# Kernel optimization log

Measured on AMD Instinct MI355X. Metric: run time of the kernel, lower is better.

## Reference

```python
import jax, jax.numpy as jnp
import numpy as np

EMBED_DIM = 1024
NUM_HEADS = 16
HEAD_DIM = EMBED_DIM // NUM_HEADS
SCALING = HEAD_DIM ** -0.5
EPS = 1e-5


def _rope(seq_len):
    inv_freq = 1.0 / (10000.0 ** (jnp.arange(0, HEAD_DIM, 2, dtype=jnp.float32) / HEAD_DIM))
    freqs = jnp.arange(seq_len, dtype=jnp.float32)[:, None] * inv_freq[None, :]
    emb = jnp.concatenate([freqs, freqs], axis=-1)  # (S, HEAD_DIM)
    return jnp.cos(emb), jnp.sin(emb)


def _rotate(x, cos, sin):
    # x: (B,H,S,Dh), cos/sin: (S,Dh)
    d = x.shape[-1]
    x1, x2 = x[..., : d // 2], x[..., d // 2 :]
    rotated = jnp.concatenate([-x2, x1], axis=-1)
    return x * cos + rotated * sin


def setup_inputs() -> dict:
    key = jax.random.key(0)
    ks = jax.random.split(key, 6)
    B, S, D = 2, 2048, EMBED_DIM
    scale = D ** -0.5
    return {
        "x": jax.random.normal(ks[0], (B, S, D), jnp.float32),
        "Wq": jax.random.normal(ks[1], (D, D), jnp.float32) * scale,
        "Wk": jax.random.normal(ks[2], (D, D), jnp.float32) * scale,
        "Wv": jax.random.normal(ks[3], (D, D), jnp.float32) * scale,
        "Wg": jax.random.normal(ks[4], (D, D), jnp.float32) * scale,
        "Wo": jax.random.normal(ks[5], (D, D), jnp.float32) * scale,
        "gn_w": jnp.ones((D,), jnp.float32),
        "gn_b": jnp.zeros((D,), jnp.float32),
    }


def reference(x, Wq, Wk, Wv, Wg, Wo, gn_w, gn_b):
    B, S, D = x.shape
    H, Dh = NUM_HEADS, HEAD_DIM

    def split_heads(t):  # (B,S,D) -> (B,H,S,Dh)
        return t.reshape(B, S, H, Dh).transpose(0, 2, 1, 3)

    q = split_heads(x @ Wq.T)
    k = split_heads(x @ Wk.T)
    v = split_heads(x @ Wv.T)

    cos, sin = _rope(S)
    q = _rotate(q, cos, sin)
    k = _rotate(k, cos, sin)

    retention = jnp.einsum("bhsd,bhtd->bhst", q, k) * SCALING

    # multiplicative causal decay mask: gamma**(n-m) for n>=m else 0
    gammas = (1.0 - 2.0 ** (-5.0 - jnp.arange(H, dtype=jnp.float32)))  # (H,)
    diff = jnp.arange(S)[:, None] - jnp.arange(S)[None, :]             # (S,S)
    causal = diff >= 0
    decay = jnp.where(causal, gammas[:, None, None] ** jnp.maximum(diff, 0).astype(jnp.float32), 0.0)  # (H,S,S)
    retention = retention * decay[None]

    out = jnp.einsum("bhst,bhtd->bhsd", retention, v)  # (B,H,S,Dh)
    out = out.transpose(0, 2, 1, 3).reshape(B * S, H, Dh)

    # GroupNorm with num_groups == H over channel dim D
    mean = out.mean(axis=-1, keepdims=True)
    var = out.var(axis=-1, keepdims=True)
    out = (out - mean) * jax.lax.rsqrt(var + EPS)
    out = out * gn_w.reshape(H, Dh) + gn_b.reshape(H, Dh)
    out = out.reshape(B, S, D)

    gate = jax.nn.silu(x @ Wg.T)
    return (gate * out) @ Wo.T
```

## Files before the change

### kernel.cpp

```cpp
#include <hip/hip_runtime.h>
#include <cstdint>
#include <cstddef>


typedef __attribute__((ext_vector_type(4))) float  f32x4;
typedef __attribute__((ext_vector_type(8))) short  bf16x8;
typedef __attribute__((ext_vector_type(4))) short  bf16x4v;
typedef __attribute__((ext_vector_type(2))) unsigned int u32x2;

#define MFMA_BF16 __builtin_amdgcn_mfma_f32_16x16x32_bf16

#define GLL16(gp, lp) __builtin_amdgcn_global_load_lds( \
    (const __attribute__((address_space(1))) unsigned int*)(const void*)(gp), \
    (__attribute__((address_space(3))) unsigned int*)(void*)(lp), 16, 0, 0)

__device__ __forceinline__ unsigned short f2bf(float f) {
    unsigned u = __float_as_uint(f);
    u += 0x7fffu + ((u >> 16) & 1u);
    return (unsigned short)(u >> 16);
}
__device__ __forceinline__ float bf2f(unsigned short h) {
    return __uint_as_float(((unsigned)h) << 16);
}
__device__ __forceinline__ unsigned cvt_pk_bf16(float lo, float hi) {
    unsigned r;
    asm("v_cvt_pk_bf16_f32 %0, %1, %2" : "=v"(r) : "v"(lo), "v"(hi));
    return r;
}

__global__ void convert_kernel(const float* __restrict__ x,
                               const float* __restrict__ wq, const float* __restrict__ wk,
                               const float* __restrict__ wv, const float* __restrict__ wg,
                               const float* __restrict__ wo,
                               unsigned short* __restrict__ dst) {
    const size_t total = 4194304u + 5u * 1048576u;
    for (size_t i = (size_t)blockIdx.x * blockDim.x + threadIdx.x;
         i * 4 < total; i += (size_t)gridDim.x * blockDim.x) {
        size_t e = i * 4;
        const float* src; size_t off;
        if (e < 4194304u) { src = x; off = e; }
        else {
            size_t r = e - 4194304u;
            int w = (int)(r >> 20); off = r & 1048575u;
            src = (w == 0) ? wq : (w == 1) ? wk : (w == 2) ? wv : (w == 3) ? wg : wo;
        }
        f32x4 v = *(const f32x4*)(src + off);
        unsigned short o0 = f2bf(v[0]), o1 = f2bf(v[1]), o2 = f2bf(v[2]), o3 = f2bf(v[3]);
        unsigned long long pack = (unsigned long long)o0 | ((unsigned long long)o1 << 16)
                                | ((unsigned long long)o2 << 32) | ((unsigned long long)o3 << 48);
        *(unsigned long long*)(dst + e) = pack;
    }
}

__global__ void rope_tables(float* __restrict__ cosT, float* __restrict__ sinT) {
    int i = blockIdx.x * blockDim.x + threadIdx.x;
    if (i >= 2048 * 32) return;
    int s = i >> 5, j = i & 31;
    float inv = exp2f(-(float)j * (13.287712379549449f / 32.0f));
    float ang = (float)s * inv;
    cosT[i] = cosf(ang);
    sinT[i] = sinf(ang);
}

__launch_bounds__(256, 2)
__global__ void gemm_fused(const unsigned short* __restrict__ A_x,
                           const unsigned short* __restrict__ A_a2,
                           const unsigned short* __restrict__ Wq, const unsigned short* __restrict__ Wk,
                           const unsigned short* __restrict__ Wv, const unsigned short* __restrict__ Wg,
                           const unsigned short* __restrict__ Wo,
                           const float* __restrict__ cosT, const float* __restrict__ sinT,
                           unsigned short* __restrict__ q_hm, unsigned short* __restrict__ k_hm,
                           unsigned short* __restrict__ kTs, unsigned short* __restrict__ vT,
                           unsigned short* __restrict__ gate,
                           float* __restrict__ outf,
                           int mode_base) {
    int mode = mode_base + blockIdx.z;
    const unsigned short* A = (mode == 4) ? A_a2 : A_x;
    const unsigned short* W = (mode == 0) ? Wq : (mode == 1) ? Wk :
                              (mode == 2) ? Wv : (mode == 3) ? Wg : Wo;

    __shared__ __align__(16) unsigned short Ash[128 * 64];
    __shared__ __align__(16) unsigned short Bsh[128 * 64];

    int tid = threadIdx.x;
    int lane = tid & 63, wid = tid >> 6;
    int wm = wid >> 1, wn = wid & 1;
    int m0 = blockIdx.y * 128, n0 = blockIdx.x * 128;

    int l_row = lane >> 3;
    int l_src = ((lane & 7) ^ l_row) << 3;
    const unsigned short* Ab = A + (size_t)(m0 + wid * 32 + l_row) * 1024 + l_src;
    const unsigned short* Wb = W + (size_t)(n0 + wid * 32 + l_row) * 1024 + l_src;

    f32x4 acc[4][4];
#pragma unroll
    for (int i = 0; i < 4; ++i)
#pragma unroll
        for (int j = 0; j < 4; ++j)
#pragma unroll
            for (int r = 0; r < 4; ++r) acc[i][j][r] = 0.0f;

    for (int k0 = 0; k0 < 1024; k0 += 64) {
        __syncthreads();
#pragma unroll
        for (int i = 0; i < 4; ++i) {
            GLL16(Ab + (size_t)(i * 8) * 1024 + k0, &Ash[(wid * 32 + i * 8) * 64]);
            GLL16(Wb + (size_t)(i * 8) * 1024 + k0, &Bsh[(wid * 32 + i * 8) * 64]);
        }
        __syncthreads();
#pragma unroll
        for (int ks = 0; ks < 2; ++ks) {
            bf16x8 af[4], bfv[4];
#pragma unroll
            for (int mi = 0; mi < 4; ++mi) {
                int row = wm * 64 + mi * 16 + (lane & 15);
                int c = ks * 4 + (lane >> 4);
                af[mi] = *(const bf16x8*)&Ash[row * 64 + ((c ^ (row & 7)) << 3)];
            }
#pragma unroll
            for (int ni = 0; ni < 4; ++ni) {
                int row = wn * 64 + ni * 16 + (lane & 15);
                int c = ks * 4 + (lane >> 4);
                bfv[ni] = *(const bf16x8*)&Bsh[row * 64 + ((c ^ (row & 7)) << 3)];
            }
            if (mode == 2) {
#pragma unroll
                for (int mi = 0; mi < 4; ++mi)
#pragma unroll
                    for (int ni = 0; ni < 4; ++ni)
                        acc[mi][ni] = MFMA_BF16(bfv[ni], af[mi], acc[mi][ni], 0, 0, 0);
            } else {
#pragma unroll
                for (int mi = 0; mi < 4; ++mi)
#pragma unroll
                    for (int ni = 0; ni < 4; ++ni)
                        acc[mi][ni] = MFMA_BF16(af[mi], bfv[ni], acc[mi][ni], 0, 0, 0);
            }
        }
    }

    int mbase = m0 + wm * 64, nbase = n0 + wn * 64;
    int g4 = (lane >> 4) << 2;

    if (mode == 0 || mode == 1) {
        unsigned short* dst = (mode == 0) ? q_hm : k_hm;
        float sr[4] = {1.f, 1.f, 1.f, 1.f}, m16p[4] = {1.f, 1.f, 1.f, 1.f};
        if (mode == 1) {
            float lg = log2f(1.0f - exp2f(-5.0f - (float)(nbase >> 6)));
            float gm1 = exp2f(-lg), gm16 = exp2f(-16.0f * lg);
            sr[0] = exp2f(lg * (float)(63 - g4));
            sr[1] = sr[0] * gm1; sr[2] = sr[1] * gm1; sr[3] = sr[2] * gm1;
            m16p[1] = gm16; m16p[2] = gm16 * gm16; m16p[3] = m16p[2] * gm16;
        }
#pragma unroll
        for (int mi = 0; mi < 4; ++mi)
#pragma unroll
            for (int ni = 0; ni < 4; ++ni)
#pragma unroll
                for (int r = 0; r < 4; ++r) {
                    int m = mbase + mi * 16 + g4 + r;
                    int n = nbase + ni * 16 + (lane & 15);
                    int s = m & 2047, b = m >> 11, h = n >> 6, d = n & 63, j = d & 31;
                    float v  = acc[mi][ni][r];
                    float v2 = acc[mi][ni ^ 2][r];
                    float cs = cosT[s * 32 + j], sn = sinT[s * 32 + j];
                    float rot = (d < 32) ? -v2 : v2;
                    float o = v * cs + rot * sn;
                    dst[((size_t)(b * 16 + h) * 2048 + s) * 64 + d] = f2bf(o);
                    if (mode == 1) {
                        kTs[((size_t)((b * 16 + h) * 64 + d)) * 2048 + s]
                            = f2bf(o * (sr[r] * m16p[mi]));
                    }
                }
    } else if (mode == 2) {
#pragma unroll
        for (int mi = 0; mi < 4; ++mi)
#pragma unroll
            for (int ni = 0; ni < 4; ++ni)
#pragma unroll
                for (int r = 0; r < 4; ++r) {
                    int n = nbase + ni * 16 + g4 + r;
                    int m = mbase + mi * 16 + (lane & 15);
                    int b = m >> 11, s = m & 2047, h = n >> 6, d = n & 63;
                    vT[((size_t)((b * 16 + h) * 64 + d)) * 2048 + s] = f2bf(acc[mi][ni][r]);
                }
    } else if (mode == 3) {
#pragma unroll
        for (int mi = 0; mi < 4; ++mi)
#pragma unroll
            for (int ni = 0; ni < 4; ++ni)
#pragma unroll
                for (int r = 0; r < 4; ++r) {
                    int m = mbase + mi * 16 + g4 + r;
                    int n = nbase + ni * 16 + (lane & 15);
                    float v = acc[mi][ni][r];
                    gate[(size_t)m * 1024 + n] = f2bf(v / (1.0f + expf(-v)));
                }
    } else {
#pragma unroll
        for (int mi = 0; mi < 4; ++mi)
#pragma unroll
            for (int ni = 0; ni < 4; ++ni)
#pragma unroll
                for (int r = 0; r < 4; ++r) {
                    int m = mbase + mi * 16 + g4 + r;
                    int n = nbase + ni * 16 + (lane & 15);
                    outf[(size_t)m * 1024 + n] = acc[mi][ni][r];
                }
    }
}

__launch_bounds__(256, 4)
__global__ void chunk_state_kernel(const unsigned short* __restrict__ vT,
                                   const unsigned short* __restrict__ kTs,
                                   unsigned short* __restrict__ LT) {
    int tid = threadIdx.x, lane = tid & 63, wid = tid >> 6;
    int bh = blockIdx.x >> 3;
    int c  = (blockIdx.x & 7) * 4 + wid;
    int q_lane = lane & 15;
    int g4 = (lane >> 4) << 2, g8 = (lane >> 4) << 3;

    const unsigned short* vb = vT  + (size_t)bh * 131072 + (size_t)c * 64;
    const unsigned short* kb = kTs + (size_t)bh * 131072 + (size_t)c * 64;

    f32x4 acc[4][4];
#pragma unroll
    for (int i = 0; i < 4; ++i)
#pragma unroll
        for (int j = 0; j < 4; ++j)
#pragma unroll
            for (int r = 0; r < 4; ++r) acc[i][j][r] = 0.0f;

#pragma unroll
    for (int ks = 0; ks < 2; ++ks) {
        bf16x8 a[4], bv[4];
#pragma unroll
        for (int mi = 0; mi < 4; ++mi)
            a[mi] = *(const bf16x8*)(vb + (size_t)(mi * 16 + q_lane) * 2048 + ks * 32 + g8);
#pragma unroll
        for (int ni = 0; ni < 4; ++ni)
            bv[ni] = *(const bf16x8*)(kb + (size_t)(ni * 16 + q_lane) * 2048 + ks * 32 + g8);
#pragma unroll
        for (int mi = 0; mi < 4; ++mi)
#pragma unroll
            for (int ni = 0; ni < 4; ++ni)
                acc[mi][ni] = MFMA_BF16(a[mi], bv[ni], acc[mi][ni], 0, 0, 0);
    }

    unsigned short* lp = LT + ((size_t)(bh * 32 + c)) * 4096;
#pragma unroll
    for (int mi = 0; mi < 4; ++mi)
#pragma unroll
        for (int ni = 0; ni < 4; ++ni)
#pragma unroll
            for (int r = 0; r < 4; ++r) {
                int d2 = mi * 16 + g4 + r;
                int d1 = ni * 16 + q_lane;
                lp[d2 * 64 + d1] = f2bf(acc[mi][ni][r]);
            }
}

__launch_bounds__(256, 4)
__global__ void scan_kernel(const unsigned short* __restrict__ LT,
                            unsigned short* __restrict__ ST) {
    int bh = blockIdx.x >> 2;
    int e0 = ((blockIdx.x & 3) * 256 + threadIdx.x) * 4;
    int h = bh & 15;
    float lg2g = log2f(1.0f - exp2f(-5.0f - (float)h));
    float g64 = exp2f(64.0f * lg2g);

    float s0 = 0.f, s1 = 0.f, s2 = 0.f, s3 = 0.f;
    const unsigned short* lp = LT + (size_t)bh * 32 * 4096 + e0;
    unsigned short* sp = ST + (size_t)bh * 32 * 4096 + e0;
    for (int c = 0; c < 32; ++c) {
        u32x2 wv;
        wv[0] = cvt_pk_bf16(s0, s1);
        wv[1] = cvt_pk_bf16(s2, s3);
        *(u32x2*)sp = wv;
        bf16x4v lv = *(const bf16x4v*)lp;
        s0 = s0 * g64 + bf2f((unsigned short)lv[0]);
        s1 = s1 * g64 + bf2f((unsigned short)lv[1]);
        s2 = s2 * g64 + bf2f((unsigned short)lv[2]);
        s3 = s3 * g64 + bf2f((unsigned short)lv[3]);
        lp += 4096; sp += 4096;
    }
}

__launch_bounds__(256, 4)
__global__ void retention_chunk_kernel(const unsigned short* __restrict__ qh,
                                       const unsigned short* __restrict__ kh,
                                       const unsigned short* __restrict__ vT,
                                       const unsigned short* __restrict__ ST,
                                       const float* __restrict__ gn_w, const float* __restrict__ gn_b,
                                       const unsigned short* __restrict__ gate,
                                       unsigned short* __restrict__ a2) {
    __shared__ __align__(16) unsigned short Ssh[4][16 * 40];

    int tid = threadIdx.x, lane = tid & 63, wid = tid >> 6;
    int c = blockIdx.x, bh = blockIdx.y;
    int b = bh >> 4, h = bh & 15;

    float lg2g = log2f(1.0f - exp2f(-5.0f - (float)h));
    float gam1 = exp2f(lg2g);
    float gmr1 = exp2f(-lg2g);
    float gmr2 = gmr1 * gmr1, gmr3 = gmr2 * gmr1;
    float gmr16 = exp2f(-16.0f * lg2g);

    int q_lane = lane & 15;
    int g4 = (lane >> 4) << 2, g8 = (lane >> 4) << 3;
    int i_col = wid * 16 + q_lane;
    int s_abs = c * 64 + i_col;

    bf16x8 aq0, aq1;
    {
        const unsigned short* qp = qh + ((size_t)bh * 2048 + s_abs) * 64 + g8;
        aq0 = *(const bf16x8*)(qp);
        aq1 = *(const bf16x8*)(qp + 32);
    }

    f32x4 z4 = {0.f, 0.f, 0.f, 0.f};
    f32x4 o0, o1, o2, o3;

    {
        const unsigned short* stp = ST + ((size_t)(bh * 32 + c)) * 4096
                                  + (size_t)q_lane * 64 + g8;
        bf16x8 s00 = *(const bf16x8*)(stp);
        bf16x8 s01 = *(const bf16x8*)(stp + 32);
        bf16x8 s10 = *(const bf16x8*)(stp + 1024);
        bf16x8 s11 = *(const bf16x8*)(stp + 1056);
        bf16x8 s20 = *(const bf16x8*)(stp + 2048);
        bf16x8 s21 = *(const bf16x8*)(stp + 2080);
        bf16x8 s30 = *(const bf16x8*)(stp + 3072);
        bf16x8 s31 = *(const bf16x8*)(stp + 3104);
        o0 = MFMA_BF16(aq0, s00, z4, 0, 0, 0); o0 = MFMA_BF16(aq1, s01, o0, 0, 0, 0);
        o1 = MFMA_BF16(aq0, s10, z4, 0, 0, 0); o1 = MFMA_BF16(aq1, s11, o1, 0, 0, 0);
        o2 = MFMA_BF16(aq0, s20, z4, 0, 0, 0); o2 = MFMA_BF16(aq1, s21, o2, 0, 0, 0);
        o3 = MFMA_BF16(aq0, s30, z4, 0, 0, 0); o3 = MFMA_BF16(aq1, s31, o3, 0, 0, 0);
    }
    {
        float cs0 = 0.125f * exp2f(lg2g * (float)(wid * 16 + g4 + 1));
        float cs1 = cs0 * gam1, cs2 = cs1 * gam1, cs3 = cs2 * gam1;
        o0[0] *= cs0; o0[1] *= cs1; o0[2] *= cs2; o0[3] *= cs3;
        o1[0] *= cs0; o1[1] *= cs1; o1[2] *= cs2; o1[3] *= cs3;
        o2[0] *= cs0; o2[1] *= cs1; o2[2] *= cs2; o2[3] *= cs3;
        o3[0] *= cs0; o3[1] *= cs1; o3[2] *= cs2; o3[3] *= cs3;
    }

    const unsigned short* kbase = kh + ((size_t)bh * 2048 + c * 64) * 64;
    const unsigned short* vbase = vT + (size_t)bh * 131072 + c * 64;
    unsigned short* ssw = &Ssh[wid][0];
    int ntt = (wid >> 1) + 1;
    for (int tt = 0; tt < ntt; ++tt) {
        int tbase = tt * 32;
        const unsigned short* kp = kbase + (size_t)(tbase + q_lane) * 64 + g8;
        bf16x8 k00 = *(const bf16x8*)(kp);
        bf16x8 k01 = *(const bf16x8*)(kp + 32);
        bf16x8 k10 = *(const bf16x8*)(kp + 1024);
        bf16x8 k11 = *(const bf16x8*)(kp + 1056);
        f32x4 sc0 = z4, sc1 = z4;
        sc0 = MFMA_BF16(k00, aq0, sc0, 0, 0, 0);
        sc0 = MFMA_BF16(k01, aq1, sc0, 0, 0, 0);
        sc1 = MFMA_BF16(k10, aq0, sc1, 0, 0, 0);
        sc1 = MFMA_BF16(k11, aq1, sc1, 0, 0, 0);

        int j0 = tbase + g4;
        float e0 = 0.125f * exp2f(lg2g * (float)(i_col - j0));
        float e1 = e0 * gmr1, e2 = e0 * gmr2, e3 = e0 * gmr3;
        float v00 = (i_col >= j0    ) ? sc0[0] * e0 : 0.0f;
        float v01 = (i_col >= j0 + 1) ? sc0[1] * e1 : 0.0f;
        float v02 = (i_col >= j0 + 2) ? sc0[2] * e2 : 0.0f;
        float v03 = (i_col >= j0 + 3) ? sc0[3] * e3 : 0.0f;
        int j1 = j0 + 16;
        float f0 = e0 * gmr16, f1 = e1 * gmr16, f2 = e2 * gmr16, f3 = e3 * gmr16;
        float v10 = (i_col >= j1    ) ? sc1[0] * f0 : 0.0f;
        float v11 = (i_col >= j1 + 1) ? sc1[1] * f1 : 0.0f;
        float v12 = (i_col >= j1 + 2) ? sc1[2] * f2 : 0.0f;
        float v13 = (i_col >= j1 + 3) ? sc1[3] * f3 : 0.0f;

        u32x2 wA, wB;
        wA[0] = cvt_pk_bf16(v00, v01); wA[1] = cvt_pk_bf16(v02, v03);
        wB[0] = cvt_pk_bf16(v10, v11); wB[1] = cvt_pk_bf16(v12, v13);
        *(u32x2*)&ssw[q_lane * 40 + g4] = wA;
        *(u32x2*)&ssw[q_lane * 40 + 16 + g4] = wB;

        bf16x8 sf = *(const bf16x8*)&ssw[q_lane * 40 + g8];
        bf16x8 bv0 = *(const bf16x8*)(vbase + (size_t)(q_lane) * 2048 + tbase + g8);
        bf16x8 bv1 = *(const bf16x8*)(vbase + (size_t)(16 + q_lane) * 2048 + tbase + g8);
        bf16x8 bv2 = *(const bf16x8*)(vbase + (size_t)(32 + q_lane) * 2048 + tbase + g8);
        bf16x8 bv3 = *(const bf16x8*)(vbase + (size_t)(48 + q_lane) * 2048 + tbase + g8);
        o0 = MFMA_BF16(sf, bv0, o0, 0, 0, 0);
        o1 = MFMA_BF16(sf, bv1, o1, 0, 0, 0);
        o2 = MFMA_BF16(sf, bv2, o2, 0, 0, 0);
        o3 = MFMA_BF16(sf, bv3, o3, 0, 0, 0);
    }

    float mean[4], rstd[4];
#pragma unroll
    for (int r = 0; r < 4; ++r) {
        float s1 = o0[r] + o1[r] + o2[r] + o3[r];
        float s2 = o0[r]*o0[r] + o1[r]*o1[r] + o2[r]*o2[r] + o3[r]*o3[r];
#pragma unroll
        for (int m = 1; m < 16; m <<= 1) {
            s1 += __shfl_xor(s1, m);
            s2 += __shfl_xor(s2, m);
        }
        float mu = s1 * 0.015625f;
        mean[r] = mu;
        float var = s2 * 0.015625f - mu * mu;
        rstd[r] = rsqrtf(var + 1e-5f);
    }
    int srow = c * 64 + wid * 16;
#define RT_STORE(OV, DB)                                                    \
    {                                                                       \
        int d = DB * 16 + q_lane;                                           \
        float gw = gn_w[h * 64 + d];                                        \
        float gb = gn_b[h * 64 + d];                                        \
        _Pragma("unroll")                                                   \
        for (int r = 0; r < 4; ++r) {                                       \
            int s_out = srow + g4 + r;                                      \
            size_t gi = ((size_t)(b * 2048 + s_out)) * 1024 + h * 64 + d;   \
            float val = (OV[r] - mean[r]) * rstd[r] * gw + gb;              \
            val *= bf2f(gate[gi]);                                          \
            a2[gi] = f2bf(val);                                             \
        }                                                                   \
    }
    RT_STORE(o0, 0); RT_STORE(o1, 1); RT_STORE(o2, 2); RT_STORE(o3, 3);
#undef RT_STORE
}

extern "C" void kernel_launch(void* const* d_in, const int* in_sizes, int n_in,
                              void* d_out, int out_size, void* d_ws, size_t ws_size,
                              hipStream_t stream) {
    const float* x    = (const float*)d_in[0];
    const float* Wq   = (const float*)d_in[1];
    const float* Wk   = (const float*)d_in[2];
    const float* Wv   = (const float*)d_in[3];
    const float* Wg   = (const float*)d_in[4];
    const float* Wo   = (const float*)d_in[5];
    const float* gn_w = (const float*)d_in[6];
    const float* gn_b = (const float*)d_in[7];

    unsigned short* xb   = (unsigned short*)d_ws;
    unsigned short* wqb  = xb  + 4194304;
    unsigned short* wkb  = wqb + 1048576;
    unsigned short* wvb  = wkb + 1048576;
    unsigned short* wgb  = wvb + 1048576;
    unsigned short* wob  = wgb + 1048576;
    float*          cosT = (float*)(wob + 1048576);
    float*          sinT = cosT + 65536;
    unsigned short* q_hm = (unsigned short*)(sinT + 65536);
    unsigned short* k_hm = q_hm + 4194304;
    unsigned short* vTb  = k_hm + 4194304;
    unsigned short* kTs  = vTb + 4194304;
    unsigned short* a2   = kTs + 4194304;
    unsigned short* gate = a2  + 4194304;
    unsigned short* LT   = a2;
    unsigned short* ST   = xb;

    float* outf = (float*)d_out;

    convert_kernel<<<dim3(2048), dim3(256), 0, stream>>>(x, Wq, Wk, Wv, Wg, Wo, xb);
    rope_tables<<<dim3(256), dim3(256), 0, stream>>>(cosT, sinT);
    gemm_fused<<<dim3(8, 32, 4), dim3(256), 0, stream>>>(
        xb, a2, wqb, wkb, wvb, wgb, wob, cosT, sinT,
        q_hm, k_hm, kTs, vTb, gate, outf, 0);
    chunk_state_kernel<<<dim3(256), dim3(256), 0, stream>>>(vTb, kTs, LT);
    scan_kernel<<<dim3(128), dim3(256), 0, stream>>>(LT, ST);
    retention_chunk_kernel<<<dim3(32, 32), dim3(256), 0, stream>>>(
        q_hm, k_hm, vTb, ST, gn_w, gn_b, gate, a2);
    gemm_fused<<<dim3(8, 32, 1), dim3(256), 0, stream>>>(
        xb, a2, wqb, wkb, wvb, wgb, wob, cosT, sinT,
        q_hm, k_hm, kTs, vTb, gate, outf, 4);
}
```

Measured before the change: 120.3 us.

## Double-buffer GEMM LDS tiles and fold rope table generation into convert kernel

The projection GEMM now ping-pongs two LDS buffers, so the global-to-LDS loads for the next K tile are issued before the MFMAs on the current tile, and there is one barrier per iteration instead of two. MFMA sections are wrapped in s_setprio to favour the math waves. Separately, the rope cos/sin table computation moves into the first 256 blocks of the convert kernel, which removes one kernel launch. Doubling LDS to 64KB per block may limit how many blocks fit per CU alongside the launch bound of 2.

After: 120.2 us, median of 2. Within noise of the previous version (-0.1%).

```diff
diff --git a/kernel.cpp b/kernel.cpp
--- a/kernel.cpp
+++ b/kernel.cpp
@@ -32,7 +32,8 @@
                                const float* __restrict__ wq, const float* __restrict__ wk,
                                const float* __restrict__ wv, const float* __restrict__ wg,
                                const float* __restrict__ wo,
-                               unsigned short* __restrict__ dst) {
+                               unsigned short* __restrict__ dst,
+                               float* __restrict__ cosT, float* __restrict__ sinT) {
     const size_t total = 4194304u + 5u * 1048576u;
     for (size_t i = (size_t)blockIdx.x * blockDim.x + threadIdx.x;
          i * 4 < total; i += (size_t)gridDim.x * blockDim.x) {
@@ -50,16 +51,14 @@
                                 | ((unsigned long long)o2 << 32) | ((unsigned long long)o3 << 48);
         *(unsigned long long*)(dst + e) = pack;
     }
-}
-
-__global__ void rope_tables(float* __restrict__ cosT, float* __restrict__ sinT) {
-    int i = blockIdx.x * blockDim.x + threadIdx.x;
-    if (i >= 2048 * 32) return;
-    int s = i >> 5, j = i & 31;
-    float inv = exp2f(-(float)j * (13.287712379549449f / 32.0f));
-    float ang = (float)s * inv;
-    cosT[i] = cosf(ang);
-    sinT[i] = sinf(ang);
+    if (blockIdx.x < 256) {
+        int i = blockIdx.x * 256 + threadIdx.x;
+        int s = i >> 5, j = i & 31;
+        float inv = exp2f(-(float)j * (13.287712379549449f / 32.0f));
+        float ang = (float)s * inv;
+        cosT[i] = cosf(ang);
+        sinT[i] = sinf(ang);
+    }
 }
 
 __launch_bounds__(256, 2)
@@ -79,8 +78,8 @@
     const unsigned short* W = (mode == 0) ? Wq : (mode == 1) ? Wk :
                               (mode == 2) ? Wv : (mode == 3) ? Wg : Wo;
 
-    __shared__ __align__(16) unsigned short Ash[128 * 64];
-    __shared__ __align__(16) unsigned short Bsh[128 * 64];
+    __shared__ __align__(16) unsigned short Ash[2][128 * 64];
+    __shared__ __align__(16) unsigned short Bsh[2][128 * 64];
 
     int tid = threadIdx.x;
     int lane = tid & 63, wid = tid >> 6;
@@ -100,44 +99,61 @@
 #pragma unroll
             for (int r = 0; r < 4; ++r) acc[i][j][r] = 0.0f;
 
-    for (int k0 = 0; k0 < 1024; k0 += 64) {
+#define STAGE(BUF, K0)                                                          \
+    _Pragma("unroll")                                                           \
+    for (int i_ = 0; i_ < 4; ++i_) {                                            \
+        GLL16(Ab + (size_t)(i_ * 8) * 1024 + (K0), &Ash[BUF][(wid * 32 + i_ * 8) * 64]); \
+        GLL16(Wb + (size_t)(i_ * 8) * 1024 + (K0), &Bsh[BUF][(wid * 32 + i_ * 8) * 64]); \
+    }
+
+#define COMPUTE(BUF)                                                            \
+    _Pragma("unroll")                                                           \
+    for (int ks = 0; ks < 2; ++ks) {                                            \
+        bf16x8 af[4], bfv[4];                                                   \
+        _Pragma("unroll")                                                       \
+        for (int mi = 0; mi < 4; ++mi) {                                        \
+            int row = wm * 64 + mi * 16 + (lane & 15);                          \
+            int c = ks * 4 + (lane >> 4);                                       \
+            af[mi] = *(const bf16x8*)&Ash[BUF][row * 64 + ((c ^ (row & 7)) << 3)]; \
+        }                                                                       \
+        _Pragma("unroll")                                                       \
+        for (int ni = 0; ni < 4; ++ni) {                                        \
+            int row = wn * 64 + ni * 16 + (lane & 15);                          \
+            int c = ks * 4 + (lane >> 4);                                       \
+            bfv[ni] = *(const bf16x8*)&Bsh[BUF][row * 64 + ((c ^ (row & 7)) << 3)]; \
+        }                                                                       \
+        __builtin_amdgcn_s_setprio(1);                                          \
+        if (mode == 2) {                                \
+            _Pragma("unroll")                                                   \
+            for (int mi = 0; mi < 4; ++mi)                                      \
+                _Pragma("unroll")                                               \
+                for (int ni = 0; ni < 4; ++ni)                                  \
+                    acc[mi][ni] = MFMA_BF16(bfv[ni], af[mi], acc[mi][ni], 0, 0, 0); \
+        } else {                                                                \
+            _Pragma("unroll")                                                   \
+            for (int mi = 0; mi < 4; ++mi)                                      \
+                _Pragma("unroll")                                               \
+                for (int ni = 0; ni < 4; ++ni)                                  \
+                    acc[mi][ni] = MFMA_BF16(af[mi], bfv[ni], acc[mi][ni], 0, 0, 0); \
+        }                                                                       \
+        __builtin_amdgcn_s_setprio(0);                                          \
+    }
+
+    STAGE(0, 0)
+    asm volatile("s_waitcnt vmcnt(0)" ::: "memory");
+    __syncthreads();
+
+    for (int t = 0; t < 15; ++t) {
+        int cur = t & 1;
+        STAGE(cur ^ 1, (t + 1) * 64)
+        COMPUTE(cur)
+        asm volatile("s_waitcnt vmcnt(0)" ::: "memory");
         __syncthreads();
-#pragma unroll
-        for (int i = 0; i < 4; ++i) {
-            GLL16(Ab + (size_t)(i * 8) * 1024 + k0, &Ash[(wid * 32 + i * 8) * 64]);
-            GLL16(Wb + (size_t)(i * 8) * 1024 + k0, &Bsh[(wid * 32 + i * 8) * 64]);
-        }
-        __syncthreads();
-#pragma unroll
-        for (int ks = 0; ks < 2; ++ks) {
-            bf16x8 af[4], bfv[4];
-#pragma unroll
-            for (int mi = 0; mi < 4; ++mi) {
-                int row = wm * 64 + mi * 16 + (lane & 15);
-                int c = ks * 4 + (lane >> 4);
-                af[mi] = *(const bf16x8*)&Ash[row * 64 + ((c ^ (row & 7)) << 3)];
-            }
-#pragma unroll
-            for (int ni = 0; ni < 4; ++ni) {
-                int row = wn * 64 + ni * 16 + (lane & 15);
-                int c = ks * 4 + (lane >> 4);
-                bfv[ni] = *(const bf16x8*)&Bsh[row * 64 + ((c ^ (row & 7)) << 3)];
-            }
-            if (mode == 2) {
-#pragma unroll
-                for (int mi = 0; mi < 4; ++mi)
-#pragma unroll
-                    for (int ni = 0; ni < 4; ++ni)
-                        acc[mi][ni] = MFMA_BF16(bfv[ni], af[mi], acc[mi][ni], 0, 0, 0);
-            } else {
-#pragma unroll
-                for (int mi = 0; mi < 4; ++mi)
-#pragma unroll
-                    for (int ni = 0; ni < 4; ++ni)
-                        acc[mi][ni] = MFMA_BF16(af[mi], bfv[ni], acc[mi][ni], 0, 0, 0);
-            }
-        }
-    }
+    }
+    COMPUTE(1)
+
+#undef STAGE
+#undef COMPUTE
 
     int mbase = m0 + wm * 64, nbase = n0 + wn * 64;
     int g4 = (lane >> 4) << 2;
@@ -459,8 +475,8 @@
 
     float* outf = (float*)d_out;
 
-    convert_kernel<<<dim3(2048), dim3(256), 0, stream>>>(x, Wq, Wk, Wv, Wg, Wo, xb);
-    rope_tables<<<dim3(256), dim3(256), 0, stream>>>(cosT, sinT);
+    convert_kernel<<<dim3(2048), dim3(256), 0, stream>>>(
+        x, Wq, Wk, Wv, Wg, Wo, xb, cosT, sinT);
     gemm_fused<<<dim3(8, 32, 4), dim3(256), 0, stream>>>(
         xb, a2, wqb, wkb, wvb, wgb, wob, cosT, sinT,
         q_hm, k_hm, kTs, vTb, gate, outf, 0);
```

## Double-buffer GEMM LDS loads, remap workgroups, and use narrower tiles for output projection

Applied to the files above, without the earlier changes.

The GEMM now double-buffers its LDS tiles, so global-to-LDS loads for the next K step are issued while MFMAs run on the current one, and it raises wave priority around the MFMA block. Workgroup indices are remapped flat across groups of eight, likely to spread neighbouring tiles across XCDs for better cache locality. The output projection uses a templated 128x64 tile with a 512-workgroup grid for better CU occupancy. The rope table computation is folded into the convert kernel to save a launch. Double buffering doubles LDS use, which can lower occupancy.

Result: slower. 132.3 us (+9.9%).

```diff
diff --git a/kernel.cpp b/kernel.cpp
--- a/kernel.cpp
+++ b/kernel.cpp
@@ -32,7 +32,8 @@
                                const float* __restrict__ wq, const float* __restrict__ wk,
                                const float* __restrict__ wv, const float* __restrict__ wg,
                                const float* __restrict__ wo,
-                               unsigned short* __restrict__ dst) {
+                               unsigned short* __restrict__ dst,
+                               float* __restrict__ cosT, float* __restrict__ sinT) {
     const size_t total = 4194304u + 5u * 1048576u;
     for (size_t i = (size_t)blockIdx.x * blockDim.x + threadIdx.x;
          i * 4 < total; i += (size_t)gridDim.x * blockDim.x) {
@@ -50,19 +51,18 @@
                                 | ((unsigned long long)o2 << 32) | ((unsigned long long)o3 << 48);
         *(unsigned long long*)(dst + e) = pack;
     }
-}
-
-__global__ void rope_tables(float* __restrict__ cosT, float* __restrict__ sinT) {
-    int i = blockIdx.x * blockDim.x + threadIdx.x;
-    if (i >= 2048 * 32) return;
-    int s = i >> 5, j = i & 31;
-    float inv = exp2f(-(float)j * (13.287712379549449f / 32.0f));
-    float ang = (float)s * inv;
-    cosT[i] = cosf(ang);
-    sinT[i] = sinf(ang);
-}
-
-__launch_bounds__(256, 2)
+    if (blockIdx.x < 256) {
+        int i = blockIdx.x * 256 + threadIdx.x;
+        int s = i >> 5, j = i & 31;
+        float inv = exp2f(-(float)j * (13.287712379549449f / 32.0f));
+        float ang = (float)s * inv;
+        cosT[i] = cosf(ang);
+        sinT[i] = sinf(ang);
+    }
+}
+
+template<int NI>
+__launch_bounds__(256, NI == 4 ? 2 : 3)
 __global__ void gemm_fused(const unsigned short* __restrict__ A_x,
                            const unsigned short* __restrict__ A_a2,
                            const unsigned short* __restrict__ Wq, const unsigned short* __restrict__ Wk,
@@ -74,133 +74,167 @@
                            unsigned short* __restrict__ gate,
                            float* __restrict__ outf,
                            int mode_base) {
-    int mode = mode_base + blockIdx.z;
+    constexpr int BROWS = NI * 32;
+
+    int flat = (blockIdx.z * gridDim.y + blockIdx.y) * gridDim.x + blockIdx.x;
+    int nwg  = gridDim.z * gridDim.y * gridDim.x;
+    int L    = (flat & 7) * (nwg >> 3) + (flat >> 3);
+
+    int mode, m0, n0;
+    if (NI == 4) {
+        mode = mode_base + (L >> 8);
+        int rem = L & 255;
+        m0 = (rem >> 3) * 128;
+        n0 = (rem & 7) * 128;
+    } else {
+        mode = mode_base;
+        m0 = (L >> 4) * 128;
+        n0 = (L & 15) * 64;
+    }
+
     const unsigned short* A = (mode == 4) ? A_a2 : A_x;
     const unsigned short* W = (mode == 0) ? Wq : (mode == 1) ? Wk :
                               (mode == 2) ? Wv : (mode == 3) ? Wg : Wo;
 
-    __shared__ __align__(16) unsigned short Ash[128 * 64];
-    __shared__ __align__(16) unsigned short Bsh[128 * 64];
+    __shared__ __align__(16) unsigned short Ash[2][128 * 64];
+    __shared__ __align__(16) unsigned short Bsh[2][BROWS * 64];
 
     int tid = threadIdx.x;
     int lane = tid & 63, wid = tid >> 6;
     int wm = wid >> 1, wn = wid & 1;
-    int m0 = blockIdx.y * 128, n0 = blockIdx.x * 128;
 
     int l_row = lane >> 3;
     int l_src = ((lane & 7) ^ l_row) << 3;
     const unsigned short* Ab = A + (size_t)(m0 + wid * 32 + l_row) * 1024 + l_src;
-    const unsigned short* Wb = W + (size_t)(n0 + wid * 32 + l_row) * 1024 + l_src;
-
-    f32x4 acc[4][4];
+    const unsigned short* Wb = W + (size_t)(n0 + wid * (BROWS / 4) + l_row) * 1024 + l_src;
+
+    f32x4 acc[4][NI];
 #pragma unroll
     for (int i = 0; i < 4; ++i)
 #pragma unroll
-        for (int j = 0; j < 4; ++j)
+        for (int j = 0; j < NI; ++j)
 #pragma unroll
             for (int r = 0; r < 4; ++r) acc[i][j][r] = 0.0f;
 
-    for (int k0 = 0; k0 < 1024; k0 += 64) {
-        __syncthreads();
-#pragma unroll
-        for (int i = 0; i < 4; ++i) {
-            GLL16(Ab + (size_t)(i * 8) * 1024 + k0, &Ash[(wid * 32 + i * 8) * 64]);
-            GLL16(Wb + (size_t)(i * 8) * 1024 + k0, &Bsh[(wid * 32 + i * 8) * 64]);
-        }
-        __syncthreads();
+    auto stage = [&](int buf, int k0) {
+#pragma unroll
+        for (int i = 0; i < 4; ++i)
+            GLL16(Ab + (size_t)(i * 8) * 1024 + k0, &Ash[buf][(wid * 32 + i * 8) * 64]);
+#pragma unroll
+        for (int i = 0; i < NI; ++i)
+            GLL16(Wb + (size_t)(i * 8) * 1024 + k0, &Bsh[buf][(wid * (BROWS / 4) + i * 8) * 64]);
+    };
+
+    auto compute = [&](int buf) {
 #pragma unroll
         for (int ks = 0; ks < 2; ++ks) {
-            bf16x8 af[4], bfv[4];
+            bf16x8 af[4], bfv[NI];
+            int c = ks * 4 + (lane >> 4);
 #pragma unroll
             for (int mi = 0; mi < 4; ++mi) {
                 int row = wm * 64 + mi * 16 + (lane & 15);
-                int c = ks * 4 + (lane >> 4);
-                af[mi] = *(const bf16x8*)&Ash[row * 64 + ((c ^ (row & 7)) << 3)];
+                af[mi] = *(const bf16x8*)&Ash[buf][row * 64 + ((c ^ (row & 7)) << 3)];
             }
 #pragma unroll
-            for (int ni = 0; ni < 4; ++ni) {
-                int row = wn * 64 + ni * 16 + (lane & 15);
-                int c = ks * 4 + (lane >> 4);
-                bfv[ni] = *(const bf16x8*)&Bsh[row * 64 + ((c ^ (row & 7)) << 3)];
+            for (int ni = 0; ni < NI; ++ni) {
+                int row = wn * (BROWS / 2) + ni * 16 + (lane & 15);
+                bfv[ni] = *(const bf16x8*)&Bsh[buf][row * 64 + ((c ^ (row & 7)) << 3)];
             }
+            __builtin_amdgcn_s_setprio(1);
             if (mode == 2) {
 #pragma unroll
                 for (int mi = 0; mi < 4; ++mi)
 #pragma unroll
-                    for (int ni = 0; ni < 4; ++ni)
+                    for (int ni = 0; ni < NI; ++ni)
                         acc[mi][ni] = MFMA_BF16(bfv[ni], af[mi], acc[mi][ni], 0, 0, 0);
             } else {
 #pragma unroll
                 for (int mi = 0; mi < 4; ++mi)
 #pragma unroll
-                    for (int ni = 0; ni < 4; ++ni)
+                    for (int ni = 0; ni < NI; ++ni)
                         acc[mi][ni] = MFMA_BF16(af[mi], bfv[ni], acc[mi][ni], 0, 0, 0);
             }
+            __builtin_amdgcn_s_setprio(0);
         }
-    }
-
-    int mbase = m0 + wm * 64, nbase = n0 + wn * 64;
+    };
+
+    stage(0, 0);
+    asm volatile("s_waitcnt vmcnt(0)" ::: "memory");
+    __syncthreads();
+
+    for (int t = 0; t < 15; ++t) {
+        int cur = t & 1;
+        stage(cur ^ 1, (t + 1) * 64);
+        compute(cur);
+        asm volatile("s_waitcnt vmcnt(0)" ::: "memory");
+        __syncthreads();
+    }
+    compute(1);
+
+    int mbase = m0 + wm * 64, nbase = n0 + wn * (BROWS / 2);
     int g4 = (lane >> 4) << 2;
 
-    if (mode == 0 || mode == 1) {
-        unsigned short* dst = (mode == 0) ? q_hm : k_hm;
-        float sr[4] = {1.f, 1.f, 1.f, 1.f}, m16p[4] = {1.f, 1.f, 1.f, 1.f};
-        if (mode == 1) {
-            float lg = log2f(1.0f - exp2f(-5.0f - (float)(nbase >> 6)));
-            float gm1 = exp2f(-lg), gm16 = exp2f(-16.0f * lg);
-            sr[0] = exp2f(lg * (float)(63 - g4));
-            sr[1] = sr[0] * gm1; sr[2] = sr[1] * gm1; sr[3] = sr[2] * gm1;
-            m16p[1] = gm16; m16p[2] = gm16 * gm16; m16p[3] = m16p[2] * gm16;
+    if constexpr (NI == 4) {
+        if (mode == 0 || mode == 1) {
+            unsigned short* dst = (mode == 0) ? q_hm : k_hm;
+            float sr[4] = {1.f, 1.f, 1.f, 1.f}, m16p[4] = {1.f, 1.f, 1.f, 1.f};
+            if (mode == 1) {
+                float lg = log2f(1.0f - exp2f(-5.0f - (float)(nbase >> 6)));
+                float gm1 = exp2f(-lg), gm16 = exp2f(-16.0f * lg);
+                sr[0] = exp2f(lg * (float)(63 - g4));
+                sr[1] = sr[0] * gm1; sr[2] = sr[1] * gm1; sr[3] = sr[2] * gm1;
+                m16p[1] = gm16; m16p[2] = gm16 * gm16; m16p[3] = m16p[2] * gm16;
+            }
+#pragma unroll
+            for (int mi = 0; mi < 4; ++mi)
+#pragma unroll
+                for (int ni = 0; ni < 4; ++ni)
+#pragma unroll
+                    for (int r = 0; r < 4; ++r) {
+                        int m = mbase + mi * 16 + g4 + r;
+                        int n = nbase + ni * 16 + (lane & 15);
+                        int s = m & 2047, b = m >> 11, h = n >> 6, d = n & 63, j = d & 31;
+                        float v  = acc[mi][ni][r];
+                        float v2 = acc[mi][ni ^ 2][r];
+                        float cs = cosT[s * 32 + j], sn = sinT[s * 32 + j];
+                        float rot = (d < 32) ? -v2 : v2;
+                        float o = v * cs + rot * sn;
+                        dst[((size_t)(b * 16 + h) * 2048 + s) * 64 + d] = f2bf(o);
+                        if (mode == 1) {
+                            kTs[((size_t)((b * 16 + h) * 64 + d)) * 2048 + s]
+                                = f2bf(o * (sr[r] * m16p[mi]));
+                        }
+                    }
+        } else if (mode == 2) {
+#pragma unroll
+            for (int mi = 0; mi < 4; ++mi)
+#pragma unroll
+                for (int ni = 0; ni < 4; ++ni)
+#pragma unroll
+                    for (int r = 0; r < 4; ++r) {
+                        int n = nbase + ni * 16 + g4 + r;
+                        int m = mbase + mi * 16 + (lane & 15);
+                        int b = m >> 11, s = m & 2047, h = n >> 6, d = n & 63;
+                        vT[((size_t)((b * 16 + h) * 64 + d)) * 2048 + s] = f2bf(acc[mi][ni][r]);
+                    }
+        } else {
+#pragma unroll
+            for (int mi = 0; mi < 4; ++mi)
+#pragma unroll
+                for (int ni = 0; ni < 4; ++ni)
+#pragma unroll
+                    for (int r = 0; r < 4; ++r) {
+                        int m = mbase + mi * 16 + g4 + r;
+                        int n = nbase + ni * 16 + (lane & 15);
+                        float v = acc[mi][ni][r];
+                        gate[(size_t)m * 1024 + n] = f2bf(v / (1.0f + expf(-v)));
+                    }
         }
+    } else {
 #pragma unroll
         for (int mi = 0; mi < 4; ++mi)
 #pragma unroll
-            for (int ni = 0; ni < 4; ++ni)
-#pragma unroll
-                for (int r = 0; r < 4; ++r) {
-                    int m = mbase + mi * 16 + g4 + r;
-                    int n = nbase + ni * 16 + (lane & 15);
-                    int s = m & 2047, b = m >> 11, h = n >> 6, d = n & 63, j = d & 31;
-                    float v  = acc[mi][ni][r];
-                    float v2 = acc[mi][ni ^ 2][r];
-                    float cs = cosT[s * 32 + j], sn = sinT[s * 32 + j];
-                    float rot = (d < 32) ? -v2 : v2;
-                    float o = v * cs + rot * sn;
-                    dst[((size_t)(b * 16 + h) * 2048 + s) * 64 + d] = f2bf(o);
-                    if (mode == 1) {
-                        kTs[((size_t)((b * 16 + h) * 64 + d)) * 2048 + s]
-                            = f2bf(o * (sr[r] * m16p[mi]));
-                    }
-                }
-    } else if (mode == 2) {
-#pragma unroll
-        for (int mi = 0; mi < 4; ++mi)
-#pragma unroll
-            for (int ni = 0; ni < 4; ++ni)
-#pragma unroll
-                for (int r = 0; r < 4; ++r) {
-                    int n = nbase + ni * 16 + g4 + r;
-                    int m = mbase + mi * 16 + (lane & 15);
-                    int b = m >> 11, s = m & 2047, h = n >> 6, d = n & 63;
-                    vT[((size_t)((b * 16 + h) * 64 + d)) * 2048 + s] = f2bf(acc[mi][ni][r]);
-                }
-    } else if (mode == 3) {
-#pragma unroll
-        for (int mi = 0; mi < 4; ++mi)
-#pragma unroll
-            for (int ni = 0; ni < 4; ++ni)
-#pragma unroll
-                for (int r = 0; r < 4; ++r) {
-                    int m = mbase + mi * 16 + g4 + r;
-                    int n = nbase + ni * 16 + (lane & 15);
-                    float v = acc[mi][ni][r];
-                    gate[(size_t)m * 1024 + n] = f2bf(v / (1.0f + expf(-v)));
-                }
-    } else {
-#pragma unroll
-        for (int mi = 0; mi < 4; ++mi)
-#pragma unroll
-            for (int ni = 0; ni < 4; ++ni)
+            for (int ni = 0; ni < NI; ++ni)
 #pragma unroll
                 for (int r = 0; r < 4; ++r) {
                     int m = mbase + mi * 16 + g4 + r;
@@ -459,16 +493,16 @@
 
     float* outf = (float*)d_out;
 
-    convert_kernel<<<dim3(2048), dim3(256), 0, stream>>>(x, Wq, Wk, Wv, Wg, Wo, xb);
-    rope_tables<<<dim3(256), dim3(256), 0, stream>>>(cosT, sinT);
-    gemm_fused<<<dim3(8, 32, 4), dim3(256), 0, stream>>>(
+    convert_kernel<<<dim3(2048), dim3(256), 0, stream>>>(
+        x, Wq, Wk, Wv, Wg, Wo, xb, cosT, sinT);
+    gemm_fused<4><<<dim3(8, 32, 4), dim3(256), 0, stream>>>(
         xb, a2, wqb, wkb, wvb, wgb, wob, cosT, sinT,
         q_hm, k_hm, kTs, vTb, gate, outf, 0);
     chunk_state_kernel<<<dim3(256), dim3(256), 0, stream>>>(vTb, kTs, LT);
     scan_kernel<<<dim3(128), dim3(256), 0, stream>>>(LT, ST);
     retention_chunk_kernel<<<dim3(32, 32), dim3(256), 0, stream>>>(
         q_hm, k_hm, vTb, ST, gn_w, gn_b, gate, a2);
-    gemm_fused<<<dim3(8, 32, 1), dim3(256), 0, stream>>>(
+    gemm_fused<2><<<dim3(16, 32, 1), dim3(256), 0, stream>>>(
         xb, a2, wqb, wkb, wvb, wgb, wob, cosT, sinT,
         q_hm, k_hm, kTs, vTb, gate, outf, 4);
 }
```
